# Performance work log

Hardware: AMD Instinct MI355X
Metric: run time of the kernel (lower is better)

## Reference

```python
import jax, jax.numpy as jnp
import numpy as np

NUM_STAGES = 4
NUM_CODEBOOKS = 1024  # 2**vq_bitrate_per_stage
DATA_DIM = 256
BEAM = 4
N = 4096
EPS = 1e-12


def setup_inputs() -> dict:
    key = jax.random.key(0)
    k1, k2, k3 = jax.random.split(key, 3)
    x = jax.random.normal(k1, (N, DATA_DIM), jnp.float32)
    # codebooks initialized Uniform(-1/K, 1/K) as in torch __init__
    cb = jax.random.uniform(k2, (NUM_STAGES * NUM_CODEBOOKS, DATA_DIM), jnp.float32,
                            -1.0 / NUM_CODEBOOKS, 1.0 / NUM_CODEBOOKS)
    rv = jax.random.normal(k3, (N, DATA_DIM), jnp.float32)
    return {"input_data": x, "codebooks": cb, "random_vector": rv, "train_mode": 1}


def _beam_search(x, codebooks):
    """Returns best_tuples [N, S]: per-sample global codebook indices, one per stage slot."""
    B, D = x.shape
    S, K, W = NUM_STAGES, NUM_CODEBOOKS, BEAM
    cb2 = jnp.sum(codebooks ** 2, axis=1)  # [S*K]

    def dists(q):  # [..., D] -> [..., S*K] squared euclidean
        return jnp.sum(q ** 2, axis=-1, keepdims=True) - 2.0 * (q @ codebooks.T) + cb2

    stage_of = jnp.arange(S * K) // K  # stage id of each flat codebook row

    # stage 0: top-BEAM nearest entries over all stages
    idx0 = jax.lax.top_k(-dists(x), W)[1].astype(jnp.int32)  # [B, W]
    tuples = jnp.full((B, W, S), -1, jnp.int32).at[:, :, 0].set(idx0)

    for it in range(S - 1):
        # Faithful to source: vq_and_remainder loop subtracts codebooks[tuples[:,:,it]]
        # (it+1) times (the loop passes iter_number, not i).
        c_it = codebooks[tuples[:, :, it]]                      # [B, W, D]
        remainder = x[:, None, :] - (it + 1) * c_it             # [B, W, D]
        # stages already used by each beam (mask via NaN-codebooks in source == +inf here)
        used = tuples[:, :, :it + 1] // K                       # [B, W, it+1]
        banned = (used[:, :, :, None] == jnp.arange(S)).any(axis=2)  # [B, W, S]
        d = dists(remainder)                                    # [B, W, S*K]
        d = jnp.where(banned[:, :, stage_of], jnp.inf, d)
        cand = jax.lax.top_k(-d, W)[1].astype(jnp.int32)        # [B, W, W]
        prime = jnp.repeat(tuples[:, :, None, :], W, axis=2)    # [B, W, W, S]
        prime = prime.at[:, :, :, it + 1].set(cand).reshape(B, W * W, S)
        # mse over the (it+2) filled slots
        q = jnp.sum(codebooks[prime[:, :, :it + 2]], axis=2)    # [B, W*W, D]
        mse = jnp.mean((x[:, None, :] - q) ** 2, axis=2)        # [B, W*W]
        if it < S - 2:
            sel = jax.lax.top_k(-mse, W)[1]                     # [B, W] smallest-mse beams
            tuples = jnp.take_along_axis(prime, sel[:, :, None], axis=1)
        else:
            best = jnp.argmin(mse, axis=1)                      # [B]
            return jnp.take_along_axis(prime, best[:, None, None], axis=1)[:, 0, :]


def reference(input_data, codebooks, random_vector, train_mode):
    best = _beam_search(input_data, jax.lax.stop_gradient(codebooks))  # [N, S] int32
    quantized = jnp.sum(codebooks[best], axis=1)                       # [N, D]
    # noise substitution VQ
    nh = jnp.sqrt(jnp.sum((input_data - quantized) ** 2, axis=1, keepdims=True))
    nr = jnp.sqrt(jnp.sum(random_vector ** 2, axis=1, keepdims=True))
    nsvq = input_data + (nh / nr + EPS) * random_vector
    # codebooks_used starts at zero; +=1 at unique selected indices -> usage indicator
    used = jnp.zeros(NUM_STAGES * NUM_CODEBOOKS, jnp.int32).at[best.reshape(-1)].set(1)
    used = used.reshape(NUM_STAGES, NUM_CODEBOOKS)
    if train_mode:
        return (nsvq, used)
    return (quantized, used)
```

## Files before the change

### kernel.cpp

```cpp
#include <hip/hip_runtime.h>
#include <math.h>

#define NSTAGES 4
#define NCB     1024
#define SK      4096
#define D       256
#define BEAM_W  4
#define NB      4096
#define INFF    __builtin_huge_valf()
#define RB      128
#define CBL     256
#define BK      32
#define NCBLK   (SK / CBL)

typedef unsigned long long u64;


template <typename F>
__device__ __forceinline__ float xw84(F v) {
  float r[32];
#pragma unroll
  for (int l = 0; l < 32; ++l) r[l] = v(l);
  for (int i = 32; i < 256; i += 32)
#pragma unroll
    for (int l = 0; l < 32; ++l) r[l] = __fadd_rn(r[l], v(i + l));
  float w[8];
#pragma unroll
  for (int j = 0; j < 8; ++j)
    w[j] = __fadd_rn(__fadd_rn(__fadd_rn(r[j], r[8 + j]), r[16 + j]), r[24 + j]);
  float s0 = __fadd_rn(w[0], w[4]);
  float s1 = __fadd_rn(w[1], w[5]);
  float s2 = __fadd_rn(w[2], w[6]);
  float s3 = __fadd_rn(w[3], w[7]);
  float t0 = __fadd_rn(s0, s2);
  float t1 = __fadd_rn(s1, s3);
  return __fadd_rn(t0, t1);
}

__device__ __forceinline__ void ins4u(u64 v, u64 b[4]) {
  if (v < b[3]) {
    b[3] = v;
    if (b[3] < b[2]) { u64 t = b[2]; b[2] = b[3]; b[3] = t; }
    if (b[2] < b[1]) { u64 t = b[1]; b[1] = b[2]; b[2] = t; }
    if (b[1] < b[0]) { u64 t = b[0]; b[0] = b[1]; b[1] = t; }
  }
}

__device__ __forceinline__ u64 shflx64(u64 v, int m) {
  int lo = __shfl_xor((int)(unsigned)(v & 0xFFFFFFFFULL), m, 64);
  int hi = __shfl_xor((int)(unsigned)(v >> 32), m, 64);
  return ((u64)(unsigned)hi << 32) | (u64)(unsigned)lo;
}

__global__ __launch_bounds__(256) void cb2_pw(const float* __restrict__ cb,
                                              float* __restrict__ cb2) {
  int row = blockIdx.x * 256 + threadIdx.x;
  if (row >= SK) return;
  const float* c = cb + (size_t)row * D;
  cb2[row] = xw84([&](int d) { float t = c[d]; return __fmul_rn(t, t); });
}

__global__ __launch_bounds__(256) void s0_pw(const float* __restrict__ x,
                                             float* __restrict__ Srow) {
  int row = blockIdx.x * 256 + threadIdx.x;
  if (row >= NB) return;
  const float* xr = x + (size_t)row * D;
  Srow[row] = xw84([&](int d) { float t = xr[d]; return __fmul_rn(t, t); });
}

__global__ __launch_bounds__(256) void srow_pw(const float* __restrict__ x,
                                               const float* __restrict__ cb,
                                               const int* __restrict__ tuples,
                                               int it,
                                               float* __restrict__ Srow) {
  int row = blockIdx.x * 256 + threadIdx.x;
  if (row >= NB * BEAM_W) return;
  int s = row >> 2;
  int slot = tuples[row * NSTAGES + it];
  const float* xr = x + (size_t)s * D;
  const float* cr = cb + (size_t)slot * D;
  const float mf = (float)(it + 1);
  Srow[row] = xw84([&](int d) {
    float t = __fsub_rn(xr[d], __fmul_rn(mf, cr[d]));
    return __fmul_rn(t, t);
  });
}

__global__ __launch_bounds__(256) void transpose_rem(
    const float* __restrict__ x, const float* __restrict__ cbk,
    const int* __restrict__ tuples, int it, int isStep0, int nrows,
    float* __restrict__ AT) {
  __shared__ float tile[64][65];
  const int t = threadIdx.x;
  const int r0 = blockIdx.x * 64;
  const int d0 = blockIdx.y * 64;
  const float mf = (float)(it + 1);
  {
    int r = r0 + (t & 63);
    int db = (t >> 6) * 16;
    const float* xr;
    const float* cr = nullptr;
    if (isStep0) {
      xr = x + (size_t)r * D;
    } else {
      xr = x + (size_t)(r >> 2) * D;
      cr = cbk + (size_t)tuples[r * NSTAGES + it] * D;
    }
#pragma unroll
    for (int l = 0; l < 4; ++l) {
      float4 v = *(const float4*)&xr[d0 + db + l * 4];
      if (!isStep0) {
        float4 c = *(const float4*)&cr[d0 + db + l * 4];
        v.x = __fsub_rn(v.x, __fmul_rn(mf, c.x));
        v.y = __fsub_rn(v.y, __fmul_rn(mf, c.y));
        v.z = __fsub_rn(v.z, __fmul_rn(mf, c.z));
        v.w = __fsub_rn(v.w, __fmul_rn(mf, c.w));
      }
      tile[t & 63][db + l * 4 + 0] = v.x;
      tile[t & 63][db + l * 4 + 1] = v.y;
      tile[t & 63][db + l * 4 + 2] = v.z;
      tile[t & 63][db + l * 4 + 3] = v.w;
    }
  }
  __syncthreads();
  {
    int dd = t >> 2;
    int rb = (t & 3) * 16;
    float* orow = AT + (size_t)(d0 + dd) * nrows + r0 + rb;
#pragma unroll
    for (int l = 0; l < 4; ++l) {
      float4 v = make_float4(tile[rb + l * 4 + 0][dd], tile[rb + l * 4 + 1][dd],
                             tile[rb + l * 4 + 2][dd], tile[rb + l * 4 + 3][dd]);
      *(float4*)&orow[l * 4] = v;
    }
  }
}

__global__ __launch_bounds__(256, 2) void gemm_fused(
    const float* __restrict__ AT, const float* __restrict__ BT,
    const float* __restrict__ Srow, const float* __restrict__ cb2,
    const int* __restrict__ tuples, int it, int isStep0, int nrows,
    u64* __restrict__ pki, float* __restrict__ XCout) {
  __shared__ __align__(16) char smem[66560];
  float* AsF = (float*)smem;
  float* BsF = (float*)(smem + 16384);
  u64*   tki = (u64*)smem;
  const int tid  = threadIdx.x;
  const int wv   = tid >> 6;
  const int lane = tid & 63;
  const int tx = tid & 15, ty = tid >> 4;
  const int row0 = blockIdx.y * RB;
  const int col0 = blockIdx.x * CBL;

  const float* aSrc[4];
  const float* bSrc[8];
#pragma unroll
  for (int c = 0; c < 4; ++c) {
    int f = (wv * 4 + c) * 256 + lane * 4;
    aSrc[c] = AT + (size_t)(f >> 7) * nrows + row0 + (f & 127);
  }
#pragma unroll
  for (int c = 0; c < 8; ++c) {
    int f = (wv * 8 + c) * 256 + lane * 4;
    bSrc[c] = BT + (size_t)(f >> 8) * SK + col0 + (f & 255);
  }

  float acc[8][16];
#pragma unroll
  for (int i = 0; i < 8; ++i)
#pragma unroll
    for (int j = 0; j < 16; ++j) acc[i][j] = 0.0f;

  for (int kt = 0; kt < D; kt += BK) {
#pragma unroll
    for (int c = 0; c < 4; ++c)
      __builtin_amdgcn_global_load_lds(
          (const __attribute__((address_space(1))) void*)aSrc[c],
          (__attribute__((address_space(3))) void*)(AsF + (wv * 4 + c) * 256), 16, 0, 0);
#pragma unroll
    for (int c = 0; c < 8; ++c)
      __builtin_amdgcn_global_load_lds(
          (const __attribute__((address_space(1))) void*)bSrc[c],
          (__attribute__((address_space(3))) void*)(BsF + (wv * 8 + c) * 256), 16, 0, 0);
#pragma unroll
    for (int c = 0; c < 4; ++c) aSrc[c] += (size_t)BK * nrows;
#pragma unroll
    for (int c = 0; c < 8; ++c) bSrc[c] += (size_t)BK * SK;
    __syncthreads();

#pragma unroll 8
    for (int k = 0; k < BK; ++k) {
      float a[8], b[16];
      *(float4*)&a[0]  = *(const float4*)&AsF[k * 128 + ty * 4];
      *(float4*)&a[4]  = *(const float4*)&AsF[k * 128 + 64 + ty * 4];
      *(float4*)&b[0]  = *(const float4*)&BsF[k * 256 + tx * 4];
      *(float4*)&b[4]  = *(const float4*)&BsF[k * 256 + 64 + tx * 4];
      *(float4*)&b[8]  = *(const float4*)&BsF[k * 256 + 128 + tx * 4];
      *(float4*)&b[12] = *(const float4*)&BsF[k * 256 + 192 + tx * 4];
#pragma unroll
      for (int i = 0; i < 8; ++i)
#pragma unroll
        for (int j = 0; j < 16; ++j)
          acc[i][j] = __fmaf_rn(a[i], b[j], acc[i][j]);
    }
    __syncthreads();
  }

  if (XCout) {
#pragma unroll
    for (int i = 0; i < 8; ++i) {
      int lrow = (i & 3) + ((i >> 2) * 64) + ty * 4;
      float* xo = XCout + (size_t)(row0 + lrow) * SK + col0;
#pragma unroll
      for (int jj = 0; jj < 4; ++jj) {
        float4 v = make_float4(acc[i][jj * 4 + 0], acc[i][jj * 4 + 1],
                               acc[i][jj * 4 + 2], acc[i][jj * 4 + 3]);
        *(float4*)&xo[(jj) * 64 + tx * 4] = v;
      }
    }
  }

#pragma unroll
  for (int i = 0; i < 8; ++i) {
    int lrow = (i & 3) + ((i >> 2) * 64) + ty * 4;
    int grow = row0 + lrow;
    float S = Srow[grow];
    int banned = 0;
    if (!isStep0)
      for (int a = 0; a <= it; ++a) banned |= 1 << (tuples[grow * NSTAGES + a] >> 10);
    u64 b4[4] = {~0ULL, ~0ULL, ~0ULL, ~0ULL};
#pragma unroll
    for (int j = 0; j < 16; ++j) {
      int gcol = col0 + (j & 3) + ((j >> 2) * 64) + tx * 4;
      float key = ((banned >> (gcol >> 10)) & 1)
                      ? INFF
                      : __fadd_rn(__fsub_rn(S, __fmul_rn(2.0f, acc[i][j])), cb2[gcol]);
      ins4u(((u64)__float_as_uint(key) << 32) | (unsigned)gcol, b4);
    }
#pragma unroll
    for (int s = 0; s < 4; ++s) tki[(size_t)lrow * 65 + tx * 4 + s] = b4[s];
  }
  __syncthreads();

  if (tid < RB) {
    u64 b4[4] = {~0ULL, ~0ULL, ~0ULL, ~0ULL};
    for (int t = 0; t < 16; ++t)
#pragma unroll
      for (int s = 0; s < 4; ++s) ins4u(tki[(size_t)tid * 65 + t * 4 + s], b4);
    size_t base = ((size_t)blockIdx.x * nrows + row0 + tid) * 4;
#pragma unroll
    for (int s = 0; s < 4; ++s) pki[base + s] = b4[s];
  }
}

__global__ __launch_bounds__(256, 2) void gemm_plain(
    const float* __restrict__ AT, const float* __restrict__ BT, int nrows,
    float* __restrict__ Gout) {
  __shared__ __align__(16) float AsF[BK * 128];
  __shared__ __align__(16) float BsF[BK * 256];
  const int tid  = threadIdx.x;
  const int wv   = tid >> 6;
  const int lane = tid & 63;
  const int tx = tid & 15, ty = tid >> 4;
  const int row0 = blockIdx.y * RB;
  const int col0 = blockIdx.x * CBL;

  const float* aSrc[4];
  const float* bSrc[8];
#pragma unroll
  for (int c = 0; c < 4; ++c) {
    int f = (wv * 4 + c) * 256 + lane * 4;
    aSrc[c] = AT + (size_t)(f >> 7) * nrows + row0 + (f & 127);
  }
#pragma unroll
  for (int c = 0; c < 8; ++c) {
    int f = (wv * 8 + c) * 256 + lane * 4;
    bSrc[c] = BT + (size_t)(f >> 8) * SK + col0 + (f & 255);
  }

  float acc[8][16];
#pragma unroll
  for (int i = 0; i < 8; ++i)
#pragma unroll
    for (int j = 0; j < 16; ++j) acc[i][j] = 0.0f;

  for (int kt = 0; kt < D; kt += BK) {
#pragma unroll
    for (int c = 0; c < 4; ++c)
      __builtin_amdgcn_global_load_lds(
          (const __attribute__((address_space(1))) void*)aSrc[c],
          (__attribute__((address_space(3))) void*)(AsF + (wv * 4 + c) * 256), 16, 0, 0);
#pragma unroll
    for (int c = 0; c < 8; ++c)
      __builtin_amdgcn_global_load_lds(
          (const __attribute__((address_space(1))) void*)bSrc[c],
          (__attribute__((address_space(3))) void*)(BsF + (wv * 8 + c) * 256), 16, 0, 0);
#pragma unroll
    for (int c = 0; c < 4; ++c) aSrc[c] += (size_t)BK * nrows;
#pragma unroll
    for (int c = 0; c < 8; ++c) bSrc[c] += (size_t)BK * SK;
    __syncthreads();

#pragma unroll 8
    for (int k = 0; k < BK; ++k) {
      float a[8], b[16];
      *(float4*)&a[0]  = *(const float4*)&AsF[k * 128 + ty * 4];
      *(float4*)&a[4]  = *(const float4*)&AsF[k * 128 + 64 + ty * 4];
      *(float4*)&b[0]  = *(const float4*)&BsF[k * 256 + tx * 4];
      *(float4*)&b[4]  = *(const float4*)&BsF[k * 256 + 64 + tx * 4];
      *(float4*)&b[8]  = *(const float4*)&BsF[k * 256 + 128 + tx * 4];
      *(float4*)&b[12] = *(const float4*)&BsF[k * 256 + 192 + tx * 4];
#pragma unroll
      for (int i = 0; i < 8; ++i)
#pragma unroll
        for (int j = 0; j < 16; ++j)
          acc[i][j] = __fmaf_rn(a[i], b[j], acc[i][j]);
    }
    __syncthreads();
  }

#pragma unroll
  for (int i = 0; i < 8; ++i) {
    int lrow = (i & 3) + ((i >> 2) * 64) + ty * 4;
    float* go = Gout + (size_t)(row0 + lrow) * SK + col0;
#pragma unroll
    for (int jj = 0; jj < 4; ++jj) {
      float4 v = make_float4(acc[i][jj * 4 + 0], acc[i][jj * 4 + 1],
                             acc[i][jj * 4 + 2], acc[i][jj * 4 + 3]);
      *(float4*)&go[jj * 64 + tx * 4] = v;
    }
  }
}

__global__ __launch_bounds__(256) void key_select(
    const float* __restrict__ XC, const float* __restrict__ G,
    const float* __restrict__ Srow, const float* __restrict__ cb2,
    const float* __restrict__ x, const float* __restrict__ cb,
    int it, int* __restrict__ tuples, int* __restrict__ best) {
  const int s = blockIdx.x;
  const int t = threadIdx.x;
  const int b = t >> 6, l = t & 63;
  const int r = s * BEAM_W + b;
  __shared__ float xcs[SK];
  __shared__ int   tup_s[4][NSTAGES];
  __shared__ float msek[16];
  __shared__ int   primes[16][NSTAGES];

  for (int i = t; i < SK / 4; i += 256)
    *(float4*)&xcs[i * 4] = *(const float4*)&XC[(size_t)s * SK + i * 4];
  if (t < 16) tup_s[t >> 2][t & 3] = tuples[(s * BEAM_W + (t >> 2)) * NSTAGES + (t & 3)];
  __syncthreads();

  const float mf = (float)(it + 1);
  const float S = Srow[r];
  const int slot = tup_s[b][it];
  int banned = 0;
  for (int a = 0; a <= it; ++a) banned |= 1 << (tup_s[b][a] >> 10);
  const float* gr = G + (size_t)slot * SK;

  u64 b4[4] = {~0ULL, ~0ULL, ~0ULL, ~0ULL};
#pragma unroll 4
  for (int i = 0; i < 16; ++i) {
    int j = (i * 64 + l) * 4;
    float4 g4 = *(const float4*)&gr[j];
    float4 x4 = *(const float4*)&xcs[j];
    float4 c4 = *(const float4*)&cb2[j];
    int ban = (banned >> (j >> 10)) & 1;
    float m0 = __fsub_rn(x4.x, __fmul_rn(mf, g4.x));
    float m1 = __fsub_rn(x4.y, __fmul_rn(mf, g4.y));
    float m2 = __fsub_rn(x4.z, __fmul_rn(mf, g4.z));
    float m3 = __fsub_rn(x4.w, __fmul_rn(mf, g4.w));
    float k0 = ban ? INFF : __fadd_rn(__fsub_rn(S, __fmul_rn(2.0f, m0)), c4.x);
    float k1 = ban ? INFF : __fadd_rn(__fsub_rn(S, __fmul_rn(2.0f, m1)), c4.y);
    float k2 = ban ? INFF : __fadd_rn(__fsub_rn(S, __fmul_rn(2.0f, m2)), c4.z);
    float k3 = ban ? INFF : __fadd_rn(__fsub_rn(S, __fmul_rn(2.0f, m3)), c4.w);
    ins4u(((u64)__float_as_uint(k0) << 32) | (unsigned)(j + 0), b4);
    ins4u(((u64)__float_as_uint(k1) << 32) | (unsigned)(j + 1), b4);
    ins4u(((u64)__float_as_uint(k2) << 32) | (unsigned)(j + 2), b4);
    ins4u(((u64)__float_as_uint(k3) << 32) | (unsigned)(j + 3), b4);
  }

#pragma unroll
  for (int m = 1; m < 64; m <<= 1) {
    u64 o0 = shflx64(b4[0], m);
    u64 o1 = shflx64(b4[1], m);
    u64 o2 = shflx64(b4[2], m);
    u64 o3 = shflx64(b4[3], m);
    ins4u(o0, b4);
    ins4u(o1, b4);
    ins4u(o2, b4);
    ins4u(o3, b4);
  }

  {
    const int L = it + 2;
#pragma unroll
    for (int pi = 0; pi < 4; ++pi) {
      const int p = b * 4 + pi;
      int tpl[NSTAGES];
      for (int a = 0; a < NSTAGES; ++a) tpl[a] = tup_s[b][a];
      tpl[it + 1] = (int)(b4[pi] & 0xFFFFFFFFULL);
      if (l == 0)
        for (int a = 0; a < NSTAGES; ++a) primes[p][a] = tpl[a];
      float v[4];
#pragma unroll
      for (int m = 0; m < 4; ++m) {
        int d = l + m * 64;
        float q = cb[(size_t)tpl[0] * D + d];
        for (int a = 1; a < L; ++a) q = __fadd_rn(q, cb[(size_t)tpl[a] * D + d]);
        float dv = __fsub_rn(x[(size_t)s * D + d], q);
        v[m] = __fmul_rn(dv, dv);
      }
      float u0 = __shfl_xor(v[0], 32, 64);
      float u1 = __shfl_xor(v[1], 32, 64);
      float u2 = __shfl_xor(v[2], 32, 64);
      float u3 = __shfl_xor(v[3], 32, 64);
      float r0 = __fadd_rn(v[0], u0);
      r0 = __fadd_rn(r0, v[1]);
      r0 = __fadd_rn(r0, u1);
      r0 = __fadd_rn(r0, v[2]);
      r0 = __fadd_rn(r0, u2);
      r0 = __fadd_rn(r0, v[3]);
      r0 = __fadd_rn(r0, u3);
      float a8  = __shfl(r0, l + 8, 64);
      float a16 = __shfl(r0, l + 16, 64);
      float a24 = __shfl(r0, l + 24, 64);
      float w = __fadd_rn(__fadd_rn(__fadd_rn(r0, a8), a16), a24);
      float w0 = __shfl(w, 0, 64);
      float w1 = __shfl(w, 1, 64);
      float w2 = __shfl(w, 2, 64);
      float w3 = __shfl(w, 3, 64);
      float w4 = __shfl(w, 4, 64);
      float w5 = __shfl(w, 5, 64);
      float w6 = __shfl(w, 6, 64);
      float w7 = __shfl(w, 7, 64);
      float s0 = __fadd_rn(w0, w4);
      float s1 = __fadd_rn(w1, w5);
      float s2 = __fadd_rn(w2, w6);
      float s3 = __fadd_rn(w3, w7);
      float t0 = __fadd_rn(s0, s2);
      float t1 = __fadd_rn(s1, s3);
      float S2 = __fadd_rn(t0, t1);
      if (l == 0) msek[p] = __fmul_rn(S2, 0.00390625f);
    }
  }
  __syncthreads();

  if (t == 0) {
    if (it < NSTAGES - 2) {
      bool taken[16] = {false};
      int  newt[BEAM_W][NSTAGES];
      for (int rr2 = 0; rr2 < BEAM_W; ++rr2) {
        int bp = -1; float bk = 0.0f;
        for (int p = 0; p < 16; ++p) {
          if (taken[p]) continue;
          if (bp < 0 || msek[p] < bk) { bk = msek[p]; bp = p; }
        }
        taken[bp] = true;
        for (int a = 0; a < NSTAGES; ++a) newt[rr2][a] = primes[bp][a];
      }
      for (int rr2 = 0; rr2 < BEAM_W; ++rr2)
        for (int a = 0; a < NSTAGES; ++a)
          tuples[(s * BEAM_W + rr2) * NSTAGES + a] = newt[rr2][a];
    } else {
      int bp = 0; float bk = msek[0];
      for (int p = 1; p < 16; ++p)
        if (msek[p] < bk) { bk = msek[p]; bp = p; }
      for (int a = 0; a < NSTAGES; ++a) best[s * NSTAGES + a] = primes[bp][a];
    }
  }
}

__global__ __launch_bounds__(256) void reduce_top4(
    const u64* __restrict__ pki, int nrows, int isStep0,
    int* __restrict__ tup, int* __restrict__ cand) {
  int r = blockIdx.x * 256 + threadIdx.x;
  if (r >= nrows) return;
  u64 b4[4] = {~0ULL, ~0ULL, ~0ULL, ~0ULL};
  for (int cblk = 0; cblk < NCBLK; ++cblk) {
    size_t base = ((size_t)cblk * nrows + r) * 4;
    ins4u(pki[base + 0], b4);
    ins4u(pki[base + 1], b4);
    ins4u(pki[base + 2], b4);
    ins4u(pki[base + 3], b4);
  }
  if (isStep0) {
#pragma unroll
    for (int s = 0; s < 4; ++s)
      tup[(r * BEAM_W + s) * NSTAGES + 0] = (int)(b4[s] & 0xFFFFFFFFULL);
  } else {
#pragma unroll
    for (int s = 0; s < 4; ++s)
      cand[r * BEAM_W + s] = (int)(b4[s] & 0xFFFFFFFFULL);
  }
}

__global__ __launch_bounds__(256) void mse_select(const float* __restrict__ x,
                                                  const float* __restrict__ cb,
                                                  const int* __restrict__ cand,
                                                  int it,
                                                  int* __restrict__ tuples,
                                                  int* __restrict__ best) {
  const int s = blockIdx.x, tid = threadIdx.x;
  const int wv = tid >> 6, lane = tid & 63;
  __shared__ float buf[4][256];
  __shared__ float rr[4][32];
  __shared__ float msek[16];
  __shared__ int   primes[16][NSTAGES];
  const int L = it + 2;

  for (int pi = 0; pi < 4; ++pi) {
    const int p = wv * 4 + pi;
    const int b = p >> 2, c = p & 3;
    int tpl[NSTAGES];
    for (int a = 0; a < NSTAGES; ++a) tpl[a] = tuples[(s * BEAM_W + b) * NSTAGES + a];
    tpl[it + 1] = cand[(s * BEAM_W + b) * BEAM_W + c];
    if (lane == 0)
      for (int a = 0; a < NSTAGES; ++a) primes[p][a] = tpl[a];
    for (int d = lane; d < D; d += 64) {
      float q = cb[(size_t)tpl[0] * D + d];
      for (int a = 1; a < L; ++a) q = __fadd_rn(q, cb[(size_t)tpl[a] * D + d]);
      float v = __fsub_rn(x[(size_t)s * D + d], q);
      buf[wv][d] = __fmul_rn(v, v);
    }
    __syncthreads();
    if (lane < 32) {
      float r = buf[wv][lane];
      for (int i = 32; i < 256; i += 32) r = __fadd_rn(r, buf[wv][i + lane]);
      rr[wv][lane] = r;
    }
    __syncthreads();
    if (lane == 0) {
      float w[8];
#pragma unroll
      for (int j = 0; j < 8; ++j)
        w[j] = __fadd_rn(__fadd_rn(__fadd_rn(rr[wv][j], rr[wv][8 + j]), rr[wv][16 + j]),
                         rr[wv][24 + j]);
      float s0 = __fadd_rn(w[0], w[4]);
      float s1 = __fadd_rn(w[1], w[5]);
      float s2 = __fadd_rn(w[2], w[6]);
      float s3 = __fadd_rn(w[3], w[7]);
      float t0 = __fadd_rn(s0, s2);
      float t1 = __fadd_rn(s1, s3);
      float S2 = __fadd_rn(t0, t1);
      msek[p] = __fmul_rn(S2, 0.00390625f);
    }
    __syncthreads();
  }

  if (tid == 0) {
    if (it < NSTAGES - 2) {
      bool taken[16] = {false};
      int  newt[BEAM_W][NSTAGES];
      for (int r = 0; r < BEAM_W; ++r) {
        int bp = -1; float bk = 0.0f;
        for (int p = 0; p < 16; ++p) {
          if (taken[p]) continue;
          if (bp < 0 || msek[p] < bk) { bk = msek[p]; bp = p; }
        }
        taken[bp] = true;
        for (int a = 0; a < NSTAGES; ++a) newt[r][a] = primes[bp][a];
      }
      for (int r = 0; r < BEAM_W; ++r)
        for (int a = 0; a < NSTAGES; ++a) tuples[(s * BEAM_W + r) * NSTAGES + a] = newt[r][a];
    } else {
      int bp = 0; float bk = msek[0];
      for (int p = 1; p < 16; ++p)
        if (msek[p] < bk) { bk = msek[p]; bp = p; }
      for (int a = 0; a < NSTAGES; ++a) best[s * NSTAGES + a] = primes[bp][a];
    }
  }
}

__global__ void zero_used(float* __restrict__ u) {
  int t = blockIdx.x * 256 + threadIdx.x;
  if (t < SK) u[t] = 0.0f;
}

__global__ __launch_bounds__(256) void finalize_kernel(const float* __restrict__ x,
                                                       const float* __restrict__ cb,
                                                       const float* __restrict__ rvec,
                                                       const int* __restrict__ best,
                                                       const int* __restrict__ tmode,
                                                       float* __restrict__ out) {
  const int i = blockIdx.x;
  const int t = threadIdx.x;
  __shared__ double s1[256], s2[256];
  const int b0 = best[i * 4 + 0], b1 = best[i * 4 + 1];
  const int b2 = best[i * 4 + 2], b3 = best[i * 4 + 3];
  float q = ((cb[(size_t)b0 * D + t] + cb[(size_t)b1 * D + t]) + cb[(size_t)b2 * D + t]) +
            cb[(size_t)b3 * D + t];
  float xv = x[(size_t)i * D + t];
  float rv = rvec[(size_t)i * D + t];
  float df = xv - q;
  s1[t] = (double)df * (double)df;
  s2[t] = (double)rv * (double)rv;
  __syncthreads();
  for (int off = 128; off; off >>= 1) {
    if (t < off) { s1[t] += s1[t + off]; s2[t] += s2[t + off]; }
    __syncthreads();
  }
  float nh = sqrtf((float)s1[0]);
  float nr = sqrtf((float)s2[0]);
  float ratio = nh / nr + 1e-12f;
  out[(size_t)i * D + t] = (*tmode != 0) ? (xv + ratio * rv) : q;
  if (t < 4) out[(size_t)NB * D + best[i * 4 + t]] = 1.0f;
}

extern "C" void kernel_launch(void* const* d_in, const int* in_sizes, int n_in,
                              void* d_out, int out_size, void* d_ws, size_t ws_size,
                              hipStream_t stream) {
  const float* x   = (const float*)d_in[0];
  const float* cb  = (const float*)d_in[1];
  const float* rv  = (const float*)d_in[2];
  const int*   tm  = (const int*)d_in[3];
  float*       out = (float*)d_out;

  const size_t XC_BYTES    = (size_t)NB * SK * sizeof(float);
  const size_t G_BYTES     = (size_t)SK * SK * sizeof(float);
  const size_t BT_BYTES    = (size_t)D * SK * sizeof(float);
  const size_t AT0_BYTES   = (size_t)D * NB * sizeof(float);
  const size_t ATL_BYTES   = (size_t)D * NB * BEAM_W * sizeof(float);
  const size_t PKI0_BYTES  = (size_t)NCBLK * NB * BEAM_W * sizeof(u64);
  const size_t PKIL_BYTES  = (size_t)NCBLK * NB * BEAM_W * 4 * sizeof(u64);
  const size_t S_BYTES     = (size_t)NB * BEAM_W * sizeof(float);
  const size_t CB2_BYTES   = (size_t)SK * sizeof(float);
  const size_t TUP_BYTES   = (size_t)NB * BEAM_W * NSTAGES * sizeof(int);
  const size_t CAND_BYTES  = (size_t)NB * BEAM_W * BEAM_W * sizeof(int);
  const size_t BEST_BYTES  = (size_t)NB * NSTAGES * sizeof(int);
  const size_t SMALL = S_BYTES + CB2_BYTES + TUP_BYTES + CAND_BYTES + BEST_BYTES;

  const size_t NEW_TOTAL    = XC_BYTES + G_BYTES + BT_BYTES + AT0_BYTES + PKI0_BYTES + SMALL;
  const size_t LEGACY_TOTAL = PKIL_BYTES + BT_BYTES + ATL_BYTES + SMALL;

  if (ws_size >= NEW_TOTAL) {
    char* ws = (char*)d_ws;
    float* XC   = (float*)ws;  ws += XC_BYTES;
    float* G    = (float*)ws;  ws += G_BYTES;
    float* cbT  = (float*)ws;  ws += BT_BYTES;
    float* AT   = (float*)ws;  ws += AT0_BYTES;
    u64*   pki  = (u64*)ws;    ws += PKI0_BYTES;
    float* Srow = (float*)ws;  ws += S_BYTES;
    float* cb2  = (float*)ws;  ws += CB2_BYTES;
    int*   tup  = (int*)ws;    ws += TUP_BYTES;
    int*   cand = (int*)ws;    ws += CAND_BYTES;
    int*   best = (int*)ws;

    cb2_pw<<<SK / 256, 256, 0, stream>>>(cb, cb2);
    s0_pw<<<NB / 256, 256, 0, stream>>>(x, Srow);
    transpose_rem<<<dim3(SK / 64, D / 64), 256, 0, stream>>>(cb, cb, tup, 0, 1, SK, cbT);
    transpose_rem<<<dim3(NB / 64, D / 64), 256, 0, stream>>>(x, cb, tup, 0, 1, NB, AT);

    gemm_plain<<<dim3(NCBLK, SK / RB), 256, 0, stream>>>(cbT, cbT, SK, G);

    gemm_fused<<<dim3(NCBLK, NB / RB), 256, 0, stream>>>(AT, cbT, Srow, cb2, tup, 0, 1, NB,
                                                         pki, XC);
    reduce_top4<<<NB / 256, 256, 0, stream>>>(pki, NB, 1, tup, cand);

    for (int it = 0; it < NSTAGES - 1; ++it) {
      srow_pw<<<(NB * BEAM_W) / 256, 256, 0, stream>>>(x, cb, tup, it, Srow);
      key_select<<<NB, 256, 0, stream>>>(XC, G, Srow, cb2, x, cb, it, tup, best);
    }

    zero_used<<<SK / 256, 256, 0, stream>>>(out + (size_t)NB * D);
    finalize_kernel<<<NB, 256, 0, stream>>>(x, cb, rv, best, tm, out);
    return;
  }

  if (ws_size < LEGACY_TOTAL) return;
  char* ws = (char*)d_ws;
  u64*   pki  = (u64*)ws;    ws += PKIL_BYTES;
  float* cbT  = (float*)ws;  ws += BT_BYTES;
  float* AT   = (float*)ws;  ws += ATL_BYTES;
  float* Srow = (float*)ws;  ws += S_BYTES;
  float* cb2  = (float*)ws;  ws += CB2_BYTES;
  int*   tup  = (int*)ws;    ws += TUP_BYTES;
  int*   cand = (int*)ws;    ws += CAND_BYTES;
  int*   best = (int*)ws;

  cb2_pw<<<SK / 256, 256, 0, stream>>>(cb, cb2);
  s0_pw<<<NB / 256, 256, 0, stream>>>(x, Srow);
  transpose_rem<<<dim3(SK / 64, D / 64), 256, 0, stream>>>(cb, cb, tup, 0, 1, SK, cbT);
  transpose_rem<<<dim3(NB / 64, D / 64), 256, 0, stream>>>(x, cb, tup, 0, 1, NB, AT);

  gemm_fused<<<dim3(NCBLK, NB / RB), 256, 0, stream>>>(AT, cbT, Srow, cb2, tup, 0, 1, NB,
                                                       pki, nullptr);
  reduce_top4<<<NB / 256, 256, 0, stream>>>(pki, NB, 1, tup, cand);

  for (int it = 0; it < NSTAGES - 1; ++it) {
    srow_pw<<<(NB * BEAM_W) / 256, 256, 0, stream>>>(x, cb, tup, it, Srow);
    transpose_rem<<<dim3(NB * BEAM_W / 64, D / 64), 256, 0, stream>>>(x, cb, tup, it, 0,
                                                                      NB * BEAM_W, AT);
    gemm_fused<<<dim3(NCBLK, (NB * BEAM_W) / RB), 256, 0, stream>>>(
        AT, cbT, Srow, cb2, tup, it, 0, NB * BEAM_W, pki, nullptr);
    reduce_top4<<<(NB * BEAM_W) / 256, 256, 0, stream>>>(pki, NB * BEAM_W, 0, tup, cand);
    mse_select<<<NB, 256, 0, stream>>>(x, cb, cand, it, tup, best);
  }

  zero_used<<<SK / 256, 256, 0, stream>>>(out + (size_t)NB * D);
  finalize_kernel<<<NB, 256, 0, stream>>>(x, cb, rv, best, tm, out);
}
```

Baseline: 598.7 us.

## Fuse all beam-search stages into one per-sample kernel with in-block top-k

```diff
diff --git a/kernel.cpp b/kernel.cpp
--- a/kernel.cpp
+++ b/kernel.cpp
@@ -136,6 +136,281 @@
   }
 }
 
+__global__ __launch_bounds__(256, 2) void gemm_plain(
+    const float* __restrict__ AT, const float* __restrict__ BT, int nrows,
+    float* __restrict__ Gout) {
+  __shared__ __align__(16) float AsF[BK * 128];
+  __shared__ __align__(16) float BsF[BK * 256];
+  const int tid  = threadIdx.x;
+  const int wv   = tid >> 6;
+  const int lane = tid & 63;
+  const int tx = tid & 15, ty = tid >> 4;
+  const int row0 = blockIdx.y * RB;
+  const int col0 = blockIdx.x * CBL;
+
+  const float* aSrc[4];
+  const float* bSrc[8];
+#pragma unroll
+  for (int c = 0; c < 4; ++c) {
+    int f = (wv * 4 + c) * 256 + lane * 4;
+    aSrc[c] = AT + (size_t)(f >> 7) * nrows + row0 + (f & 127);
+  }
+#pragma unroll
+  for (int c = 0; c < 8; ++c) {
+    int f = (wv * 8 + c) * 256 + lane * 4;
+    bSrc[c] = BT + (size_t)(f >> 8) * SK + col0 + (f & 255);
+  }
+
+  float acc[8][16];
+#pragma unroll
+  for (int i = 0; i < 8; ++i)
+#pragma unroll
+    for (int j = 0; j < 16; ++j) acc[i][j] = 0.0f;
+
+  for (int kt = 0; kt < D; kt += BK) {
+#pragma unroll
+    for (int c = 0; c < 4; ++c)
+      __builtin_amdgcn_global_load_lds(
+          (const __attribute__((address_space(1))) void*)aSrc[c],
+          (__attribute__((address_space(3))) void*)(AsF + (wv * 4 + c) * 256), 16, 0, 0);
+#pragma unroll
+    for (int c = 0; c < 8; ++c)
+      __builtin_amdgcn_global_load_lds(
+          (const __attribute__((address_space(1))) void*)bSrc[c],
+          (__attribute__((address_space(3))) void*)(BsF + (wv * 8 + c) * 256), 16, 0, 0);
+#pragma unroll
+    for (int c = 0; c < 4; ++c) aSrc[c] += (size_t)BK * nrows;
+#pragma unroll
+    for (int c = 0; c < 8; ++c) bSrc[c] += (size_t)BK * SK;
+    __syncthreads();
+
+#pragma unroll 8
+    for (int k = 0; k < BK; ++k) {
+      float a[8], b[16];
+      *(float4*)&a[0]  = *(const float4*)&AsF[k * 128 + ty * 4];
+      *(float4*)&a[4]  = *(const float4*)&AsF[k * 128 + 64 + ty * 4];
+      *(float4*)&b[0]  = *(const float4*)&BsF[k * 256 + tx * 4];
+      *(float4*)&b[4]  = *(const float4*)&BsF[k * 256 + 64 + tx * 4];
+      *(float4*)&b[8]  = *(const float4*)&BsF[k * 256 + 128 + tx * 4];
+      *(float4*)&b[12] = *(const float4*)&BsF[k * 256 + 192 + tx * 4];
+#pragma unroll
+      for (int i = 0; i < 8; ++i)
+#pragma unroll
+        for (int j = 0; j < 16; ++j)
+          acc[i][j] = __fmaf_rn(a[i], b[j], acc[i][j]);
+    }
+    __syncthreads();
+  }
+
+#pragma unroll
+  for (int i = 0; i < 8; ++i) {
+    int lrow = (i & 3) + ((i >> 2) * 64) + ty * 4;
+    float* go = Gout + (size_t)(row0 + lrow) * SK + col0;
+#pragma unroll
+    for (int jj = 0; jj < 4; ++jj) {
+      float4 v = make_float4(acc[i][jj * 4 + 0], acc[i][jj * 4 + 1],
+                             acc[i][jj * 4 + 2], acc[i][jj * 4 + 3]);
+      *(float4*)&go[jj * 64 + tx * 4] = v;
+    }
+  }
+}
+
+__global__ __launch_bounds__(256) void beam_full(
+    const float* __restrict__ XC, const float* __restrict__ G,
+    const float* __restrict__ Srow0, const float* __restrict__ cb2,
+    const float* __restrict__ x, const float* __restrict__ cb,
+    int* __restrict__ best) {
+  const int s = blockIdx.x;
+  const int t = threadIdx.x;
+  const int b = t >> 6, l = t & 63;
+  __shared__ float xcs[SK];
+  __shared__ int   tup_s[4][NSTAGES];
+  __shared__ float msek[16];
+  __shared__ int   primes[16][NSTAGES];
+
+  for (int i = t; i < SK / 4; i += 256)
+    *(float4*)&xcs[i * 4] = *(const float4*)&XC[(size_t)s * SK + i * 4];
+  __syncthreads();
+
+  {
+    const float S0 = Srow0[s];
+    u64 b4[4] = {~0ULL, ~0ULL, ~0ULL, ~0ULL};
+#pragma unroll 4
+    for (int i = 0; i < 16; ++i) {
+      int j = (i * 64 + l) * 4;
+      float4 x4 = *(const float4*)&xcs[j];
+      float4 c4 = *(const float4*)&cb2[j];
+      float k0 = __fadd_rn(__fsub_rn(S0, __fmul_rn(2.0f, x4.x)), c4.x);
+      float k1 = __fadd_rn(__fsub_rn(S0, __fmul_rn(2.0f, x4.y)), c4.y);
+      float k2 = __fadd_rn(__fsub_rn(S0, __fmul_rn(2.0f, x4.z)), c4.z);
+      float k3 = __fadd_rn(__fsub_rn(S0, __fmul_rn(2.0f, x4.w)), c4.w);
+      ins4u(((u64)__float_as_uint(k0) << 32) | (unsigned)(j + 0), b4);
+      ins4u(((u64)__float_as_uint(k1) << 32) | (unsigned)(j + 1), b4);
+      ins4u(((u64)__float_as_uint(k2) << 32) | (unsigned)(j + 2), b4);
+      ins4u(((u64)__float_as_uint(k3) << 32) | (unsigned)(j + 3), b4);
+    }
+#pragma unroll
+    for (int m = 1; m < 64; m <<= 1) {
+      u64 o0 = shflx64(b4[0], m);
+      u64 o1 = shflx64(b4[1], m);
+      u64 o2 = shflx64(b4[2], m);
+      u64 o3 = shflx64(b4[3], m);
+      ins4u(o0, b4);
+      ins4u(o1, b4);
+      ins4u(o2, b4);
+      ins4u(o3, b4);
+    }
+    if (l == 0) tup_s[b][0] = (int)(b4[b] & 0xFFFFFFFFULL);
+  }
+  __syncthreads();
+
+  for (int it = 0; it < NSTAGES - 1; ++it) {
+    const float mf = (float)(it + 1);
+    const int slot = tup_s[b][it];
+    int banned = 0;
+    for (int a = 0; a <= it; ++a) banned |= 1 << (tup_s[b][a] >> 10);
+
+    float S;
+    {
+      const int ll = l & 31;
+      const float* xr = x + (size_t)s * D;
+      const float* cr = cb + (size_t)slot * D;
+      float tt = __fsub_rn(xr[ll], __fmul_rn(mf, cr[ll]));
+      float rl = __fmul_rn(tt, tt);
+      for (int i = 32; i < 256; i += 32) {
+        float t2 = __fsub_rn(xr[ll + i], __fmul_rn(mf, cr[ll + i]));
+        rl = __fadd_rn(rl, __fmul_rn(t2, t2));
+      }
+      int j = l & 7;
+      float rj   = __shfl(rl, j, 64);
+      float rj8  = __shfl(rl, j + 8, 64);
+      float rj16 = __shfl(rl, j + 16, 64);
+      float rj24 = __shfl(rl, j + 24, 64);
+      float w = __fadd_rn(__fadd_rn(__fadd_rn(rj, rj8), rj16), rj24);
+      float w0 = __shfl(w, 0, 64), w1 = __shfl(w, 1, 64);
+      float w2 = __shfl(w, 2, 64), w3 = __shfl(w, 3, 64);
+      float w4 = __shfl(w, 4, 64), w5 = __shfl(w, 5, 64);
+      float w6 = __shfl(w, 6, 64), w7 = __shfl(w, 7, 64);
+      float s0 = __fadd_rn(w0, w4);
+      float s1 = __fadd_rn(w1, w5);
+      float s2 = __fadd_rn(w2, w6);
+      float s3 = __fadd_rn(w3, w7);
+      float t0 = __fadd_rn(s0, s2);
+      float t1 = __fadd_rn(s1, s3);
+      S = __fadd_rn(t0, t1);
+    }
+
+    const float* gr = G + (size_t)slot * SK;
+
+    u64 b4[4] = {~0ULL, ~0ULL, ~0ULL, ~0ULL};
+#pragma unroll 4
+    for (int i = 0; i < 16; ++i) {
+      int j = (i * 64 + l) * 4;
+      float4 g4 = *(const float4*)&gr[j];
+      float4 x4 = *(const float4*)&xcs[j];
+      float4 c4 = *(const float4*)&cb2[j];
+      int ban = (banned >> (j >> 10)) & 1;
+      float m0 = __fsub_rn(x4.x, __fmul_rn(mf, g4.x));
+      float m1 = __fsub_rn(x4.y, __fmul_rn(mf, g4.y));
+      float m2 = __fsub_rn(x4.z, __fmul_rn(mf, g4.z));
+      float m3 = __fsub_rn(x4.w, __fmul_rn(mf, g4.w));
+      float k0 = ban ? INFF : __fadd_rn(__fsub_rn(S, __fmul_rn(2.0f, m0)), c4.x);
+      float k1 = ban ? INFF : __fadd_rn(__fsub_rn(S, __fmul_rn(2.0f, m1)), c4.y);
+      float k2 = ban ? INFF : __fadd_rn(__fsub_rn(S, __fmul_rn(2.0f, m2)), c4.z);
+      float k3 = ban ? INFF : __fadd_rn(__fsub_rn(S, __fmul_rn(2.0f, m3)), c4.w);
+      ins4u(((u64)__float_as_uint(k0) << 32) | (unsigned)(j + 0), b4);
+      ins4u(((u64)__float_as_uint(k1) << 32) | (unsigned)(j + 1), b4);
+      ins4u(((u64)__float_as_uint(k2) << 32) | (unsigned)(j + 2), b4);
+      ins4u(((u64)__float_as_uint(k3) << 32) | (unsigned)(j + 3), b4);
+    }
+#pragma unroll
+    for (int m = 1; m < 64; m <<= 1) {
+      u64 o0 = shflx64(b4[0], m);
+      u64 o1 = shflx64(b4[1], m);
+      u64 o2 = shflx64(b4[2], m);
+      u64 o3 = shflx64(b4[3], m);
+      ins4u(o0, b4);
+      ins4u(o1, b4);
+      ins4u(o2, b4);
+      ins4u(o3, b4);
+    }
+
+    {
+      const int L = it + 2;
+#pragma unroll
+      for (int pi = 0; pi < 4; ++pi) {
+        const int p = b * 4 + pi;
+        int tpl[NSTAGES];
+        for (int a = 0; a < NSTAGES; ++a) tpl[a] = tup_s[b][a];
+        tpl[it + 1] = (int)(b4[pi] & 0xFFFFFFFFULL);
+        if (l == 0)
+          for (int a = 0; a < NSTAGES; ++a) primes[p][a] = tpl[a];
+        float v[4];
+#pragma unroll
+        for (int m = 0; m < 4; ++m) {
+          int d = l + m * 64;
+          float q = cb[(size_t)tpl[0] * D + d];
+          for (int a = 1; a < L; ++a) q = __fadd_rn(q, cb[(size_t)tpl[a] * D + d]);
+          float dv = __fsub_rn(x[(size_t)s * D + d], q);
+          v[m] = __fmul_rn(dv, dv);
+        }
+        float u0 = __shfl_xor(v[0], 32, 64);
+        float u1 = __shfl_xor(v[1], 32, 64);
+        float u2 = __shfl_xor(v[2], 32, 64);
+        float u3 = __shfl_xor(v[3], 32, 64);
+        float r0 = __fadd_rn(v[0], u0);
+        r0 = __fadd_rn(r0, v[1]);
+        r0 = __fadd_rn(r0, u1);
+        r0 = __fadd_rn(r0, v[2]);
+        r0 = __fadd_rn(r0, u2);
+        r0 = __fadd_rn(r0, v[3]);
+        r0 = __fadd_rn(r0, u3);
+        float a8  = __shfl(r0, l + 8, 64);
+        float a16 = __shfl(r0, l + 16, 64);
+        float a24 = __shfl(r0, l + 24, 64);
+        float w = __fadd_rn(__fadd_rn(__fadd_rn(r0, a8), a16), a24);
+        float w0 = __shfl(w, 0, 64), w1 = __shfl(w, 1, 64);
+        float w2 = __shfl(w, 2, 64), w3 = __shfl(w, 3, 64);
+        float w4 = __shfl(w, 4, 64), w5 = __shfl(w, 5, 64);
+        float w6 = __shfl(w, 6, 64), w7 = __shfl(w, 7, 64);
+        float s0 = __fadd_rn(w0, w4);
+        float s1 = __fadd_rn(w1, w5);
+        float s2 = __fadd_rn(w2, w6);
+        float s3 = __fadd_rn(w3, w7);
+        float t0 = __fadd_rn(s0, s2);
+        float t1 = __fadd_rn(s1, s3);
+        float S2 = __fadd_rn(t0, t1);
+        if (l == 0) msek[p] = __fmul_rn(S2, 0.00390625f);
+      }
+    }
+    __syncthreads();
+
+    if (t == 0) {
+      if (it < NSTAGES - 2) {
+        bool taken[16] = {false};
+        int  newt[BEAM_W][NSTAGES];
+        for (int rr2 = 0; rr2 < BEAM_W; ++rr2) {
+          int bp = -1; float bk = 0.0f;
+          for (int p = 0; p < 16; ++p) {
+            if (taken[p]) continue;
+            if (bp < 0 || msek[p] < bk) { bk = msek[p]; bp = p; }
+          }
+          taken[bp] = true;
+          for (int a = 0; a < NSTAGES; ++a) newt[rr2][a] = primes[bp][a];
+        }
+        for (int rr2 = 0; rr2 < BEAM_W; ++rr2)
+          for (int a = 0; a < NSTAGES; ++a) tup_s[rr2][a] = newt[rr2][a];
+      } else {
+        int bp = 0; float bk = msek[0];
+        for (int p = 1; p < 16; ++p)
+          if (msek[p] < bk) { bk = msek[p]; bp = p; }
+        for (int a = 0; a < NSTAGES; ++a) best[s * NSTAGES + a] = primes[bp][a];
+      }
+    }
+    __syncthreads();
+  }
+}
+
 __global__ __launch_bounds__(256, 2) void gemm_fused(
     const float* __restrict__ AT, const float* __restrict__ BT,
     const float* __restrict__ Srow, const float* __restrict__ cb2,
@@ -250,224 +525,6 @@
     size_t base = ((size_t)blockIdx.x * nrows + row0 + tid) * 4;
 #pragma unroll
     for (int s = 0; s < 4; ++s) pki[base + s] = b4[s];
-  }
-}
-
-__global__ __launch_bounds__(256, 2) void gemm_plain(
-    const float* __restrict__ AT, const float* __restrict__ BT, int nrows,
-    float* __restrict__ Gout) {
-  __shared__ __align__(16) float AsF[BK * 128];
-  __shared__ __align__(16) float BsF[BK * 256];
-  const int tid  = threadIdx.x;
-  const int wv   = tid >> 6;
-  const int lane = tid & 63;
-  const int tx = tid & 15, ty = tid >> 4;
-  const int row0 = blockIdx.y * RB;
-  const int col0 = blockIdx.x * CBL;
-
-  const float* aSrc[4];
-  const float* bSrc[8];
-#pragma unroll
-  for (int c = 0; c < 4; ++c) {
-    int f = (wv * 4 + c) * 256 + lane * 4;
-    aSrc[c] = AT + (size_t)(f >> 7) * nrows + row0 + (f & 127);
-  }
-#pragma unroll
-  for (int c = 0; c < 8; ++c) {
-    int f = (wv * 8 + c) * 256 + lane * 4;
-    bSrc[c] = BT + (size_t)(f >> 8) * SK + col0 + (f & 255);
-  }
-
-  float acc[8][16];
-#pragma unroll
-  for (int i = 0; i < 8; ++i)
-#pragma unroll
-    for (int j = 0; j < 16; ++j) acc[i][j] = 0.0f;
-
-  for (int kt = 0; kt < D; kt += BK) {
-#pragma unroll
-    for (int c = 0; c < 4; ++c)
-      __builtin_amdgcn_global_load_lds(
-          (const __attribute__((address_space(1))) void*)aSrc[c],
-          (__attribute__((address_space(3))) void*)(AsF + (wv * 4 + c) * 256), 16, 0, 0);
-#pragma unroll
-    for (int c = 0; c < 8; ++c)
-      __builtin_amdgcn_global_load_lds(
-          (const __attribute__((address_space(1))) void*)bSrc[c],
-          (__attribute__((address_space(3))) void*)(BsF + (wv * 8 + c) * 256), 16, 0, 0);
-#pragma unroll
-    for (int c = 0; c < 4; ++c) aSrc[c] += (size_t)BK * nrows;
-#pragma unroll
-    for (int c = 0; c < 8; ++c) bSrc[c] += (size_t)BK * SK;
-    __syncthreads();
-
-#pragma unroll 8
-    for (int k = 0; k < BK; ++k) {
-      float a[8], b[16];
-      *(float4*)&a[0]  = *(const float4*)&AsF[k * 128 + ty * 4];
-      *(float4*)&a[4]  = *(const float4*)&AsF[k * 128 + 64 + ty * 4];
-      *(float4*)&b[0]  = *(const float4*)&BsF[k * 256 + tx * 4];
-      *(float4*)&b[4]  = *(const float4*)&BsF[k * 256 + 64 + tx * 4];
-      *(float4*)&b[8]  = *(const float4*)&BsF[k * 256 + 128 + tx * 4];
-      *(float4*)&b[12] = *(const float4*)&BsF[k * 256 + 192 + tx * 4];
-#pragma unroll
-      for (int i = 0; i < 8; ++i)
-#pragma unroll
-        for (int j = 0; j < 16; ++j)
-          acc[i][j] = __fmaf_rn(a[i], b[j], acc[i][j]);
-    }
-    __syncthreads();
-  }
-
-#pragma unroll
-  for (int i = 0; i < 8; ++i) {
-    int lrow = (i & 3) + ((i >> 2) * 64) + ty * 4;
-    float* go = Gout + (size_t)(row0 + lrow) * SK + col0;
-#pragma unroll
-    for (int jj = 0; jj < 4; ++jj) {
-      float4 v = make_float4(acc[i][jj * 4 + 0], acc[i][jj * 4 + 1],
-                             acc[i][jj * 4 + 2], acc[i][jj * 4 + 3]);
-      *(float4*)&go[jj * 64 + tx * 4] = v;
-    }
-  }
-}
-
-__global__ __launch_bounds__(256) void key_select(
-    const float* __restrict__ XC, const float* __restrict__ G,
-    const float* __restrict__ Srow, const float* __restrict__ cb2,
-    const float* __restrict__ x, const float* __restrict__ cb,
-    int it, int* __restrict__ tuples, int* __restrict__ best) {
-  const int s = blockIdx.x;
-  const int t = threadIdx.x;
-  const int b = t >> 6, l = t & 63;
-  const int r = s * BEAM_W + b;
-  __shared__ float xcs[SK];
-  __shared__ int   tup_s[4][NSTAGES];
-  __shared__ float msek[16];
-  __shared__ int   primes[16][NSTAGES];
-
-  for (int i = t; i < SK / 4; i += 256)
-    *(float4*)&xcs[i * 4] = *(const float4*)&XC[(size_t)s * SK + i * 4];
-  if (t < 16) tup_s[t >> 2][t & 3] = tuples[(s * BEAM_W + (t >> 2)) * NSTAGES + (t & 3)];
-  __syncthreads();
-
-  const float mf = (float)(it + 1);
-  const float S = Srow[r];
-  const int slot = tup_s[b][it];
-  int banned = 0;
-  for (int a = 0; a <= it; ++a) banned |= 1 << (tup_s[b][a] >> 10);
-  const float* gr = G + (size_t)slot * SK;
-
-  u64 b4[4] = {~0ULL, ~0ULL, ~0ULL, ~0ULL};
-#pragma unroll 4
-  for (int i = 0; i < 16; ++i) {
-    int j = (i * 64 + l) * 4;
-    float4 g4 = *(const float4*)&gr[j];
-    float4 x4 = *(const float4*)&xcs[j];
-    float4 c4 = *(const float4*)&cb2[j];
-    int ban = (banned >> (j >> 10)) & 1;
-    float m0 = __fsub_rn(x4.x, __fmul_rn(mf, g4.x));
-    float m1 = __fsub_rn(x4.y, __fmul_rn(mf, g4.y));
-    float m2 = __fsub_rn(x4.z, __fmul_rn(mf, g4.z));
-    float m3 = __fsub_rn(x4.w, __fmul_rn(mf, g4.w));
-    float k0 = ban ? INFF : __fadd_rn(__fsub_rn(S, __fmul_rn(2.0f, m0)), c4.x);
-    float k1 = ban ? INFF : __fadd_rn(__fsub_rn(S, __fmul_rn(2.0f, m1)), c4.y);
-    float k2 = ban ? INFF : __fadd_rn(__fsub_rn(S, __fmul_rn(2.0f, m2)), c4.z);
-    float k3 = ban ? INFF : __fadd_rn(__fsub_rn(S, __fmul_rn(2.0f, m3)), c4.w);
-    ins4u(((u64)__float_as_uint(k0) << 32) | (unsigned)(j + 0), b4);
-    ins4u(((u64)__float_as_uint(k1) << 32) | (unsigned)(j + 1), b4);
-    ins4u(((u64)__float_as_uint(k2) << 32) | (unsigned)(j + 2), b4);
-    ins4u(((u64)__float_as_uint(k3) << 32) | (unsigned)(j + 3), b4);
-  }
-
-#pragma unroll
-  for (int m = 1; m < 64; m <<= 1) {
-    u64 o0 = shflx64(b4[0], m);
-    u64 o1 = shflx64(b4[1], m);
-    u64 o2 = shflx64(b4[2], m);
-    u64 o3 = shflx64(b4[3], m);
-    ins4u(o0, b4);
-    ins4u(o1, b4);
-    ins4u(o2, b4);
-    ins4u(o3, b4);
-  }
-
-  {
-    const int L = it + 2;
-#pragma unroll
-    for (int pi = 0; pi < 4; ++pi) {
-      const int p = b * 4 + pi;
-      int tpl[NSTAGES];
-      for (int a = 0; a < NSTAGES; ++a) tpl[a] = tup_s[b][a];
-      tpl[it + 1] = (int)(b4[pi] & 0xFFFFFFFFULL);
-      if (l == 0)
-        for (int a = 0; a < NSTAGES; ++a) primes[p][a] = tpl[a];
-      float v[4];
-#pragma unroll
-      for (int m = 0; m < 4; ++m) {
-        int d = l + m * 64;
-        float q = cb[(size_t)tpl[0] * D + d];
-        for (int a = 1; a < L; ++a) q = __fadd_rn(q, cb[(size_t)tpl[a] * D + d]);
-        float dv = __fsub_rn(x[(size_t)s * D + d], q);
-        v[m] = __fmul_rn(dv, dv);
-      }
-      float u0 = __shfl_xor(v[0], 32, 64);
-      float u1 = __shfl_xor(v[1], 32, 64);
-      float u2 = __shfl_xor(v[2], 32, 64);
-      float u3 = __shfl_xor(v[3], 32, 64);
-      float r0 = __fadd_rn(v[0], u0);
-      r0 = __fadd_rn(r0, v[1]);
-      r0 = __fadd_rn(r0, u1);
-      r0 = __fadd_rn(r0, v[2]);
-      r0 = __fadd_rn(r0, u2);
-      r0 = __fadd_rn(r0, v[3]);
-      r0 = __fadd_rn(r0, u3);
-      float a8  = __shfl(r0, l + 8, 64);
-      float a16 = __shfl(r0, l + 16, 64);
-      float a24 = __shfl(r0, l + 24, 64);
-      float w = __fadd_rn(__fadd_rn(__fadd_rn(r0, a8), a16), a24);
-      float w0 = __shfl(w, 0, 64);
-      float w1 = __shfl(w, 1, 64);
-      float w2 = __shfl(w, 2, 64);
-      float w3 = __shfl(w, 3, 64);
-      float w4 = __shfl(w, 4, 64);
-      float w5 = __shfl(w, 5, 64);
-      float w6 = __shfl(w, 6, 64);
-      float w7 = __shfl(w, 7, 64);
-      float s0 = __fadd_rn(w0, w4);
-      float s1 = __fadd_rn(w1, w5);
-      float s2 = __fadd_rn(w2, w6);
-      float s3 = __fadd_rn(w3, w7);
-      float t0 = __fadd_rn(s0, s2);
-      float t1 = __fadd_rn(s1, s3);
-      float S2 = __fadd_rn(t0, t1);
-      if (l == 0) msek[p] = __fmul_rn(S2, 0.00390625f);
-    }
-  }
-  __syncthreads();
-
-  if (t == 0) {
-    if (it < NSTAGES - 2) {
-      bool taken[16] = {false};
-      int  newt[BEAM_W][NSTAGES];
-      for (int rr2 = 0; rr2 < BEAM_W; ++rr2) {
-        int bp = -1; float bk = 0.0f;
-        for (int p = 0; p < 16; ++p) {
-          if (taken[p]) continue;
-          if (bp < 0 || msek[p] < bk) { bk = msek[p]; bp = p; }
-        }
-        taken[bp] = true;
-        for (int a = 0; a < NSTAGES; ++a) newt[rr2][a] = primes[bp][a];
-      }
-      for (int rr2 = 0; rr2 < BEAM_W; ++rr2)
-        for (int a = 0; a < NSTAGES; ++a)
-          tuples[(s * BEAM_W + rr2) * NSTAGES + a] = newt[rr2][a];
-    } else {
-      int bp = 0; float bk = msek[0];
-      for (int p = 1; p < 16; ++p)
-        if (msek[p] < bk) { bk = msek[p]; bp = p; }
-      for (int a = 0; a < NSTAGES; ++a) best[s * NSTAGES + a] = primes[bp][a];
-    }
   }
 }
 
@@ -645,6 +702,7 @@
     int*   tup  = (int*)ws;    ws += TUP_BYTES;
     int*   cand = (int*)ws;    ws += CAND_BYTES;
     int*   best = (int*)ws;
+    (void)pki; (void)cand;
 
     cb2_pw<<<SK / 256, 256, 0, stream>>>(cb, cb2);
     s0_pw<<<NB / 256, 256, 0, stream>>>(x, Srow);
@@ -652,15 +710,9 @@
     transpose_rem<<<dim3(NB / 64, D / 64), 256, 0, stream>>>(x, cb, tup, 0, 1, NB, AT);
 
     gemm_plain<<<dim3(NCBLK, SK / RB), 256, 0, stream>>>(cbT, cbT, SK, G);
-
-    gemm_fused<<<dim3(NCBLK, NB / RB), 256, 0, stream>>>(AT, cbT, Srow, cb2, tup, 0, 1, NB,
-                                                         pki, XC);
-    reduce_top4<<<NB / 256, 256, 0, stream>>>(pki, NB, 1, tup, cand);
-
-    for (int it = 0; it < NSTAGES - 1; ++it) {
-      srow_pw<<<(NB * BEAM_W) / 256, 256, 0, stream>>>(x, cb, tup, it, Srow);
-      key_select<<<NB, 256, 0, stream>>>(XC, G, Srow, cb2, x, cb, it, tup, best);
-    }
+    gemm_plain<<<dim3(NCBLK, NB / RB), 256, 0, stream>>>(AT, cbT, NB, XC);
+
+    beam_full<<<NB, 256, 0, stream>>>(XC, G, Srow, cb2, x, cb, best);
 
     zero_used<<<SK / 256, 256, 0, stream>>>(out + (size_t)NB * D);
     finalize_kernel<<<NB, 256, 0, stream>>>(x, cb, rv, best, tm, out);
```

Result: no change. 606.2 us (+1.3%).
